# Performance work log

Measured on AMD Instinct MI355X. Metric: run time of the kernel, lower is better.

Reference implementation:

```python
import jax, jax.numpy as jnp
import numpy as np

N = 16384      # query points
XD = 3         # coord dims
CD = 2         # conditioning dims
E = 4          # experts
M = 2048       # memory entries per expert
D3 = 128       # feature_dim_3d (= key_dim)
D1 = 64        # feature_dim_1d
HE = 256       # encoder mlp hidden
HM = 256       # final mlp hidden
RES = 64       # line resolution (cond_hidden_dims)
TOPK_MEM = 16  # top_K memory entries
NF = 10        # positional-encoding frequencies
OMEGA = 30.0   # siren frequency


def pos_enc(c):
    # NeRF PE, torch ordering: coords, then per-freq per-dim (sin, cos)
    outs = [c]
    for i in range(NF):
        for j in range(XD):
            a = (2.0 ** i) * np.pi * c[:, j]
            outs.append(jnp.sin(a)[:, None])
            outs.append(jnp.cos(a)[:, None])
    return jnp.concatenate(outs, axis=-1)  # [N, 63]


def layernorm(h, g, b, eps=1e-5):
    mu = jnp.mean(h, axis=-1, keepdims=True)
    var = jnp.var(h, axis=-1, keepdims=True)
    return (h - mu) * jax.lax.rsqrt(var + eps) * g + b


def setup_inputs() -> dict:
    key = jax.random.key(0)
    ks = jax.random.split(key, 32)
    nrm = lambda i, shape, s: jax.random.normal(ks[i], shape, dtype=jnp.float32) * s
    inp = {}
    inp['x'] = jax.random.uniform(ks[0], (N, XD + CD), dtype=jnp.float32)
    # lines: U(0.01**0.5, 0.02**0.5) per torch init (len(line_dimid)=2)
    inp['lines'] = jax.random.uniform(ks[1], (CD, D1, RES), minval=0.1, maxval=0.1414, dtype=jnp.float32)
    # manager net
    inp['Wm1'] = nrm(2, (XD, 64), 0.5)
    inp['bm1'] = jnp.zeros((64,), jnp.float32)
    inp['Wm2'] = nrm(3, (64, E), 0.5)
    inp['bm2'] = jnp.zeros((E,), jnp.float32)
    # per-expert siren encoder (xavier-ish)
    inp['We1'] = nrm(4, (E, 63, HE), (2.0 / (63 + HE)) ** 0.5)
    inp['be1'] = jnp.zeros((E, HE), jnp.float32)
    inp['We2'] = nrm(5, (E, HE, HE), (1.0 / HE) ** 0.5)
    inp['be2'] = jnp.zeros((E, HE), jnp.float32)
    inp['We3'] = nrm(6, (E, HE, D3), (2.0 / (HE + D3)) ** 0.5)
    inp['be3'] = jnp.zeros((E, D3), jnp.float32)
    # shared layernorm on query features
    inp['ln_g'] = jnp.ones((D3,), jnp.float32)
    inp['ln_b'] = jnp.zeros((D3,), jnp.float32)
    # per-expert cross attention
    s = D3 ** -0.5
    inp['Wq'] = nrm(7, (E, D3, D3), s)
    inp['Wk'] = nrm(8, (E, D3, D3), s)
    inp['Wv'] = nrm(9, (E, D3, D3), s)
    inp['A1'] = nrm(10, (E, D3 + D1, 64), (2.0 / (D3 + D1 + 64)) ** 0.5)
    inp['a1'] = nrm(11, (E, 64), 0.001)
    inp['A2'] = nrm(12, (E, 64, D3), (2.0 / (64 + D3)) ** 0.5)
    inp['a2'] = nrm(13, (E, D3), 0.001)
    inp['aln_g'] = jnp.ones((E, D3), jnp.float32)
    inp['aln_b'] = jnp.zeros((E, D3), jnp.float32)
    # memory banks: keys kaiming-ish, values U(-1e-3, 1e-3)
    inp['mem_k'] = nrm(14, (E, M, D3), (2.0 / D3) ** 0.5)
    inp['mem_v'] = jax.random.uniform(ks[15], (E, M, D3), minval=-0.001, maxval=0.001, dtype=jnp.float32)
    # final mlp
    inp['M1'] = nrm(16, (D3, HM), (2.0 / (D3 + HM)) ** 0.5)
    inp['c1'] = nrm(17, (HM,), 0.001)
    inp['M2'] = nrm(18, (HM, HM), (2.0 / (HM + HM)) ** 0.5)
    inp['c2'] = nrm(19, (HM,), 0.001)
    inp['M3'] = nrm(20, (HM, HM), (2.0 / (HM + HM)) ** 0.5)
    inp['c3'] = nrm(21, (HM,), 0.001)
    inp['M4'] = nrm(22, (HM, 1), (2.0 / (HM + 1)) ** 0.5)
    inp['c4'] = nrm(23, (1,), 0.001)
    inp['top_k'] = 2
    return inp


def reference(x, lines, Wm1, bm1, Wm2, bm2, We1, be1, We2, be2, We3, be3,
              ln_g, ln_b, Wq, Wk, Wv, A1, a1, A2, a2, aln_g, aln_b,
              mem_k, mem_v, M1, c1, M2, c2, M3, c3, M4, c4, top_k):
    coords = x[:, :XD]
    # --- 1D line feature product (param_feats) ---
    pf = jnp.ones((D1, x.shape[0]), x.dtype)
    for i in range(CD):
        p = x[:, XD + i] * (RES - 1)
        f = jnp.floor(p)
        w = p - f
        i0 = f.astype(jnp.int32)
        i1 = jnp.clip(f + 1.0, 0.0, RES - 1).astype(jnp.int32)
        a = lines[i][:, i0]          # [D1, N]
        b = lines[i][:, i1]
        pf = pf * (a + w * (b - a))  # torch.lerp
    param_feats = pf.T               # [N, D1]
    # --- manager gating ---
    logits = jax.nn.relu(coords @ Wm1 + bm1) @ Wm2 + bm2
    probs = jax.nn.softmax(logits, axis=-1)
    gvals, gidx = jax.lax.top_k(probs, top_k)
    gvals = gvals / jnp.sum(gvals, axis=-1, keepdims=True)
    pe = pos_enc(coords)             # [N, 63]
    scale = D3 ** 0.5
    spatial = jnp.zeros((x.shape[0], D3), x.dtype)
    for e in range(E):
        # siren encoder
        h = jnp.sin(OMEGA * (pe @ We1[e] + be1[e]))
        h = jnp.sin(OMEGA * (h @ We2[e] + be2[e]))
        feats = h @ We3[e] + be3[e]                      # [N, D3]
        q = layernorm(feats, ln_g, ln_b)
        Q = q @ Wq[e]                                    # [N, D3]
        K = mem_k[e] @ Wk[e]                             # [M, D3]
        V = mem_v[e] @ Wv[e]
        # chunked topk over unscaled scores == global topk (chunk_size >= top_K)
        scores = Q @ K.T                                 # [N, M]
        _, ti = jax.lax.top_k(scores, TOPK_MEM)          # [N, k]
        Kt = K[ti]                                       # [N, k, D3]
        Vt = V[ti]
        pf_b = jnp.broadcast_to(param_feats[:, None, :], (Vt.shape[0], TOPK_MEM, D1))
        ain = jnp.concatenate([Vt, pf_b], axis=-1)       # [N, k, D3+D1]
        ad = jax.nn.relu(ain @ A1[e] + a1[e]) @ A2[e] + a2[e]
        Va = Vt + layernorm(ad, aln_g[e], aln_b[e])
        attn = jax.nn.softmax(jnp.einsum('nd,nkd->nk', Q, Kt) / scale, axis=-1)
        out_e = jnp.einsum('nk,nkd->nd', attn, Va) + feats
        w_e = jnp.sum(jnp.where(gidx == e, gvals, 0.0), axis=-1)  # routing weight
        spatial = spatial + w_e[:, None] * out_e
    h = jax.nn.relu(spatial @ M1 + c1)
    h = jax.nn.relu(h @ M2 + c2)
    h = jax.nn.relu(h @ M3 + c3)
    return jax.nn.sigmoid(h @ M4 + c4)
```

## Files before the change

### kernel.cpp

```cpp
#include <hip/hip_runtime.h>
#include <hip/hip_bf16.h>
#include <math.h>

#define NPTS 16384
#define NE 4
#define NM 2048
#define DD 128
#define DP 64
#define NHE 256
#define NHM 256
#define NRES 64
#define NTK 16
#define NEG_INF -3.402823466e38f

typedef unsigned short u16;
typedef __attribute__((ext_vector_type(8))) short short8;
typedef __attribute__((ext_vector_type(4))) float f32x4;

__device__ __forceinline__ u16 f2bf(float x) {
  union { float f; unsigned u; } v; v.f = x;
  unsigned r = v.u + 0x7fffu + ((v.u >> 16) & 1u);
  return (u16)(r >> 16);
}
__device__ __forceinline__ float bf2f(u16 b) {
  union { float f; unsigned u; } v; v.u = ((unsigned)b) << 16;
  return v.f;
}
__device__ __forceinline__ u16 bf2mono(u16 b) {
  return (u16)(b ^ ((b & 0x8000u) ? 0xFFFFu : 0x8000u));
}
__device__ __forceinline__ u16 mono2bf(u16 m) {
  return (u16)((m & 0x8000u) ? (m ^ 0x8000u) : (m ^ 0xFFFFu));
}

__global__ __launch_bounds__(256) void k_preproc(
    const float* __restrict__ x, const float* __restrict__ lines,
    const float* __restrict__ Wm1, const float* __restrict__ bm1,
    const float* __restrict__ Wm2, const float* __restrict__ bm2,
    float* __restrict__ pf, float* __restrict__ pe,
    float* __restrict__ slotW, int* __restrict__ plist,
    int* __restrict__ pairE, int* __restrict__ pairS, int* __restrict__ cnt)
{
  int n = blockIdx.x * 256 + threadIdx.x;
  int lane = threadIdx.x & 63;
  float c0 = x[n*5+0], c1 = x[n*5+1], c2 = x[n*5+2];

  float l0 = bm2[0], l1 = bm2[1], l2 = bm2[2], l3 = bm2[3];
#pragma unroll 4
  for (int j = 0; j < 64; ++j) {
    float h = fmaf(c0, Wm1[j], fmaf(c1, Wm1[64+j], fmaf(c2, Wm1[128+j], bm1[j])));
    h = fmaxf(h, 0.f);
    l0 = fmaf(h, Wm2[j*4+0], l0);
    l1 = fmaf(h, Wm2[j*4+1], l1);
    l2 = fmaf(h, Wm2[j*4+2], l2);
    l3 = fmaf(h, Wm2[j*4+3], l3);
  }
  float lg[4] = {l0, l1, l2, l3};
  float mx = fmaxf(fmaxf(l0, l1), fmaxf(l2, l3));
  float pr[4]; float ssum = 0.f;
#pragma unroll
  for (int k = 0; k < 4; ++k) { pr[k] = expf(lg[k] - mx); ssum += pr[k]; }
#pragma unroll
  for (int k = 0; k < 4; ++k) pr[k] /= ssum;
  int i0 = 0;
#pragma unroll
  for (int k = 1; k < 4; ++k) if (pr[k] > pr[i0]) i0 = k;
  int i1 = (i0 == 0) ? 1 : 0;
#pragma unroll
  for (int k = 0; k < 4; ++k) if (k != i0 && pr[k] > pr[i1]) i1 = k;
  float g0 = pr[i0], g1 = pr[i1], gs = g0 + g1;
  g0 /= gs; g1 /= gs;

  int s0 = 0, s1 = 0;
  unsigned long long below = (1ull << lane) - 1ull;
#pragma unroll
  for (int ee = 0; ee < 4; ++ee) {
    unsigned long long m0 = __ballot(i0 == ee);
    unsigned long long m1 = __ballot(i1 == ee);
    int tot = __popcll(m0) + __popcll(m1);
    int base = 0;
    if (lane == 0 && tot > 0) base = atomicAdd(&cnt[ee], tot);
    base = __shfl(base, 0);
    if (i0 == ee) s0 = base + __popcll(m0 & below);
    if (i1 == ee) s1 = base + __popcll(m0) + __popcll(m1 & below);
  }
  plist[i0*NPTS + s0] = n; slotW[i0*NPTS + s0] = g0;
  plist[i1*NPTS + s1] = n; slotW[i1*NPTS + s1] = g1;
  pairE[n*2+0] = i0; pairE[n*2+1] = i1;
  pairS[n*2+0] = s0; pairS[n*2+1] = s1;

  pe[(size_t)n*64 + 0] = c0;
  pe[(size_t)n*64 + 1] = c1;
  pe[(size_t)n*64 + 2] = c2;
  float cc[3] = {c0, c1, c2};
#pragma unroll
  for (int i = 0; i < 10; ++i) {
    float sc = 3.14159274101257324f * (float)(1 << i);
#pragma unroll
    for (int j = 0; j < 3; ++j) {
      float a = sc * cc[j];
      pe[(size_t)n*64 + 3 + (i*3+j)*2 + 0] = sinf(a);
      pe[(size_t)n*64 + 3 + (i*3+j)*2 + 1] = cosf(a);
    }
  }
  pe[(size_t)n*64 + 63] = 0.f;

  float pfv[64];
#pragma unroll
  for (int d = 0; d < 64; ++d) pfv[d] = 1.f;
  for (int i = 0; i < 2; ++i) {
    float p = x[n*5 + 3 + i] * 63.0f;
    float f = floorf(p);
    float wfr = p - f;
    int j0 = (int)f;
    int j1 = (int)fminf(f + 1.0f, 63.0f);
    const float* L = lines + (size_t)i * 64 * 64;
#pragma unroll
    for (int d = 0; d < 64; ++d) {
      float a = L[d*64 + j0];
      float b = L[d*64 + j1];
      pfv[d] *= a + wfr * (b - a);
    }
  }
#pragma unroll
  for (int d = 0; d < 64; ++d) pf[(size_t)n*64 + d] = pfv[d];
}

__global__ __launch_bounds__(256) void k_kv(
    const float* __restrict__ mem_k, const float* __restrict__ mem_v,
    const float* __restrict__ Wk, const float* __restrict__ Wv,
    u16* __restrict__ Khf, float* __restrict__ Vhat)
{
  int e = blockIdx.y;
  int which = blockIdx.z;
  const float* src = which ? mem_v : mem_k;
  const float* W   = which ? Wv : Wk;
  int r0 = blockIdx.x * 32;
  __shared__ float sm[32][130];
  int tid = threadIdx.x;
  for (int idx = tid; idx < 32*32; idx += 256) {
    int r = idx >> 5, c4 = (idx & 31) * 4;
    float4 v = *(const float4*)(src + ((size_t)e*NM + r0 + r)*DD + c4);
    sm[r][c4+0] = v.x; sm[r][c4+1] = v.y; sm[r][c4+2] = v.z; sm[r][c4+3] = v.w;
  }
  __syncthreads();
  int r = tid >> 3, cb = (tid & 7) * 16;
  float acc[16];
#pragma unroll
  for (int i = 0; i < 16; ++i) acc[i] = 0.f;
  const float* We = W + (size_t)e*DD*DD;
#pragma unroll 4
  for (int k = 0; k < 128; ++k) {
    float s = sm[r][k];
    const float4* w4 = (const float4*)(We + (size_t)k*DD + cb);
#pragma unroll
    for (int q = 0; q < 4; ++q) {
      float4 wv = w4[q];
      acc[q*4+0] = fmaf(s, wv.x, acc[q*4+0]);
      acc[q*4+1] = fmaf(s, wv.y, acc[q*4+1]);
      acc[q*4+2] = fmaf(s, wv.z, acc[q*4+2]);
      acc[q*4+3] = fmaf(s, wv.w, acc[q*4+3]);
    }
  }
  if (which) {
    float* drow = Vhat + ((size_t)e*NM + r0 + r)*DD + cb;
#pragma unroll
    for (int i = 0; i < 16; ++i) drow[i] = acc[i];
  } else {
    int key = r0 + r;
    int T = key >> 4;
    int kr = key & 15;
#pragma unroll
    for (int b = 0; b < 2; ++b) {
      int k_off = cb + b*8;
      int kt = k_off >> 5;
      int lhi = (k_off >> 3) & 3;
      int lane_ = lhi*16 + kr;
      size_t dst = (((size_t)e*128 + T)*4 + kt)*512 + (size_t)lane_*8;
      unsigned ph[4];
#pragma unroll
      for (int p = 0; p < 4; ++p) {
        u16 h0 = f2bf(acc[b*8 + p*2 + 0]);
        u16 h1 = f2bf(acc[b*8 + p*2 + 1]);
        ph[p] = (unsigned)h0 | ((unsigned)h1 << 16);
      }
      *(uint4*)(Khf + dst) = make_uint4(ph[0], ph[1], ph[2], ph[3]);
    }
  }
}

__global__ __launch_bounds__(64) void k_pack(
    const float* __restrict__ We1, const float* __restrict__ We2,
    const float* __restrict__ We3, const float* __restrict__ Wq,
    const float* __restrict__ A1, const float* __restrict__ A2,
    u16* __restrict__ We1h, u16* __restrict__ We1l,
    u16* __restrict__ We2h, u16* __restrict__ We2l,
    u16* __restrict__ We3h, u16* __restrict__ We3l,
    u16* __restrict__ Wqh,  u16* __restrict__ Wql,
    u16* __restrict__ A1h,  u16* __restrict__ A1l,
    u16* __restrict__ A2h,  u16* __restrict__ A2l)
{
  int e = blockIdx.y;
  int f = blockIdx.x;
  int lane = threadIdx.x;
  int col = lane & 15, khalf = lane >> 4;
  const float* src; u16 *dh, *dl;
  int Krows, N, ks, ct;
  if (f < 32) {
    int fl = f;        src = We1 + (size_t)e*63*256;  Krows = 63;  N = 256;
    ks = fl >> 4; ct = fl & 15;
    dh = We1h + ((size_t)e*32  + fl)*512; dl = We1l + ((size_t)e*32  + fl)*512;
  } else if (f < 160) {
    int fl = f - 32;   src = We2 + (size_t)e*256*256; Krows = 256; N = 256;
    ks = fl >> 4; ct = fl & 15;
    dh = We2h + ((size_t)e*128 + fl)*512; dl = We2l + ((size_t)e*128 + fl)*512;
  } else if (f < 224) {
    int fl = f - 160;  src = We3 + (size_t)e*256*128; Krows = 256; N = 128;
    ks = fl >> 3; ct = fl & 7;
    dh = We3h + ((size_t)e*64  + fl)*512; dl = We3l + ((size_t)e*64  + fl)*512;
  } else if (f < 256) {
    int fl = f - 224;  src = Wq  + (size_t)e*128*128; Krows = 128; N = 128;
    ks = fl >> 3; ct = fl & 7;
    dh = Wqh  + ((size_t)e*32  + fl)*512; dl = Wql  + ((size_t)e*32  + fl)*512;
  } else if (f < 280) {
    int fl = f - 256;  src = A1  + (size_t)e*192*64;  Krows = 192; N = 64;
    ks = fl >> 2; ct = fl & 3;
    dh = A1h  + ((size_t)e*24  + fl)*512; dl = A1l  + ((size_t)e*24  + fl)*512;
  } else {
    int fl = f - 280;  src = A2  + (size_t)e*64*128;  Krows = 64;  N = 128;
    ks = fl >> 3; ct = fl & 7;
    dh = A2h  + ((size_t)e*16  + fl)*512; dl = A2l  + ((size_t)e*16  + fl)*512;
  }
  unsigned ph[4], pl[4];
#pragma unroll
  for (int p = 0; p < 4; ++p) {
    int k0 = ks*32 + khalf*8 + 2*p;
    float x0 = (k0   < Krows) ? src[(size_t)k0*N     + ct*16 + col] : 0.f;
    float x1 = (k0+1 < Krows) ? src[(size_t)(k0+1)*N + ct*16 + col] : 0.f;
    u16 h0 = f2bf(x0), h1 = f2bf(x1);
    u16 l0 = f2bf(x0 - bf2f(h0)), l1 = f2bf(x1 - bf2f(h1));
    ph[p] = (unsigned)h0 | ((unsigned)h1 << 16);
    pl[p] = (unsigned)l0 | ((unsigned)l1 << 16);
  }
  *(uint4*)(dh + lane*8) = make_uint4(ph[0], ph[1], ph[2], ph[3]);
  *(uint4*)(dl + lane*8) = make_uint4(pl[0], pl[1], pl[2], pl[3]);
}

__global__ __launch_bounds__(64) void k_packM(
    const float* __restrict__ M1, const float* __restrict__ M2,
    const float* __restrict__ M3,
    u16* __restrict__ M1h, u16* __restrict__ M1l,
    u16* __restrict__ M2h, u16* __restrict__ M2l,
    u16* __restrict__ M3h, u16* __restrict__ M3l)
{
  int f = blockIdx.x;
  int lane = threadIdx.x;
  int col = lane & 15, khalf = lane >> 4;
  const float* src; u16 *dh, *dl;
  int ks, ct;
  if (f < 64)       { int fl=f;     src=M1; ks=fl>>4; ct=fl&15; dh=M1h+(size_t)fl*512; dl=M1l+(size_t)fl*512; }
  else if (f < 192) { int fl=f-64;  src=M2; ks=fl>>4; ct=fl&15; dh=M2h+(size_t)fl*512; dl=M2l+(size_t)fl*512; }
  else              { int fl=f-192; src=M3; ks=fl>>4; ct=fl&15; dh=M3h+(size_t)fl*512; dl=M3l+(size_t)fl*512; }
  unsigned ph[4], pl[4];
#pragma unroll
  for (int p = 0; p < 4; ++p) {
    int k0 = ks*32 + khalf*8 + 2*p;
    float x0 = src[(size_t)k0*NHM     + ct*16 + col];
    float x1 = src[(size_t)(k0+1)*NHM + ct*16 + col];
    u16 h0 = f2bf(x0), h1 = f2bf(x1);
    u16 l0 = f2bf(x0 - bf2f(h0)), l1 = f2bf(x1 - bf2f(h1));
    ph[p] = (unsigned)h0 | ((unsigned)h1 << 16);
    pl[p] = (unsigned)l0 | ((unsigned)l1 << 16);
  }
  *(uint4*)(dh + lane*8) = make_uint4(ph[0], ph[1], ph[2], ph[3]);
  *(uint4*)(dl + lane*8) = make_uint4(pl[0], pl[1], pl[2], pl[3]);
}

#define CONV_FRAG(PTR, AH, AL) {                                        \
    const float* p_ = (PTR);                                            \
    float4 u0_ = *(const float4*)p_, u1_ = *(const float4*)(p_+4);      \
    float xv_[8] = {u0_.x,u0_.y,u0_.z,u0_.w,u1_.x,u1_.y,u1_.z,u1_.w};   \
    union { unsigned u[4]; short8 s; } H_, L_;                          \
    _Pragma("unroll")                                                   \
    for (int q_ = 0; q_ < 4; ++q_) {                                    \
      u16 h0_ = f2bf(xv_[2*q_]), h1_ = f2bf(xv_[2*q_+1]);               \
      u16 l0_ = f2bf(xv_[2*q_] - bf2f(h0_));                            \
      u16 l1_ = f2bf(xv_[2*q_+1] - bf2f(h1_));                          \
      H_.u[q_] = (unsigned)h0_ | ((unsigned)h1_ << 16);                 \
      L_.u[q_] = (unsigned)l0_ | ((unsigned)l1_ << 16);                 \
    }                                                                   \
    AH = H_.s; AL = L_.s; }

__global__ __launch_bounds__(256) void k_expert(
    const float* __restrict__ pe,
    const u16* __restrict__ We1h, const u16* __restrict__ We1l,
    const u16* __restrict__ We2h, const u16* __restrict__ We2l,
    const u16* __restrict__ We3h, const u16* __restrict__ We3l,
    const u16* __restrict__ Wqh,  const u16* __restrict__ Wql,
    const float* __restrict__ be1, const float* __restrict__ be2,
    const float* __restrict__ be3,
    const float* __restrict__ ln_g, const float* __restrict__ ln_b,
    const int* __restrict__ plist, const int* __restrict__ cnt,
    float* __restrict__ featsC, float* __restrict__ QC)
{
  int e = blockIdx.y;
  int count = cnt[e];
  int base = blockIdx.x * 32;
  if (base >= count) return;
  __shared__ float actA[16*512];
  __shared__ float lnS[256];
  __shared__ int pts[32];
  int tid = threadIdx.x;
  int w = tid >> 6, lane = tid & 63;
  int rloc = lane & 15, khalf = lane >> 4;

  if (tid < 32) {
    int slot = base + tid;
    pts[tid] = (slot < count) ? plist[e*NPTS + slot] : 0;
  } else if (tid >= 64 && tid < 192) {
    int i = tid - 64;
    lnS[i] = ln_g[i];
    lnS[128 + i] = ln_b[i];
  }
  __syncthreads();
  {
    int Mt = tid >> 7, ks = (tid >> 6) & 1;
    const float* src = pe + (size_t)pts[Mt*16 + rloc]*64 + ks*32 + khalf*8;
    float4 a = *(const float4*)src;
    float4 b = *(const float4*)(src + 4);
    float* d = &actA[(Mt*8 + ks)*512 + lane*8];
    *(float4*)d = a; *(float4*)(d + 4) = b;
  }
  __syncthreads();

  {
    f32x4 acc[2][4];
#pragma unroll
    for (int Mt = 0; Mt < 2; ++Mt)
#pragma unroll
      for (int c = 0; c < 4; ++c) acc[Mt][c] = (f32x4){0.f,0.f,0.f,0.f};
    for (int ks = 0; ks < 2; ++ks) {
      short8 ah[2], al[2];
#pragma unroll
      for (int Mt = 0; Mt < 2; ++Mt)
        CONV_FRAG(&actA[(Mt*8+ks)*512 + lane*8], ah[Mt], al[Mt]);
#pragma unroll
      for (int c = 0; c < 4; ++c) {
        size_t fo = ((size_t)e*32 + ks*16 + w*4 + c)*512 + (size_t)lane*8;
        short8 bh = *(const short8*)(We1h + fo);
        short8 bl = *(const short8*)(We1l + fo);
#pragma unroll
        for (int Mt = 0; Mt < 2; ++Mt) {
          acc[Mt][c] = __builtin_amdgcn_mfma_f32_16x16x32_bf16(ah[Mt], bh, acc[Mt][c], 0,0,0);
          acc[Mt][c] = __builtin_amdgcn_mfma_f32_16x16x32_bf16(ah[Mt], bl, acc[Mt][c], 0,0,0);
          acc[Mt][c] = __builtin_amdgcn_mfma_f32_16x16x32_bf16(al[Mt], bh, acc[Mt][c], 0,0,0);
        }
      }
    }
    __syncthreads();
#pragma unroll
    for (int Mt = 0; Mt < 2; ++Mt)
#pragma unroll
      for (int c = 0; c < 4; ++c) {
        int n = (w*4+c)*16 + rloc;
        float b = be1[e*NHE + n];
        int ksp = n >> 5, lp = ((n>>3)&3)*16, jp = n & 7;
#pragma unroll
        for (int i = 0; i < 4; ++i)
          actA[(Mt*8+ksp)*512 + (lp + khalf*4 + i)*8 + jp] = sinf(30.f*(acc[Mt][c][i] + b));
      }
    __syncthreads();
  }

  {
    f32x4 acc[2][4];
#pragma unroll
    for (int Mt = 0; Mt < 2; ++Mt)
#pragma unroll
      for (int c = 0; c < 4; ++c) acc[Mt][c] = (f32x4){0.f,0.f,0.f,0.f};
#pragma unroll 2
    for (int ks = 0; ks < 8; ++ks) {
      short8 ah[2], al[2];
#pragma unroll
      for (int Mt = 0; Mt < 2; ++Mt)
        CONV_FRAG(&actA[(Mt*8+ks)*512 + lane*8], ah[Mt], al[Mt]);
#pragma unroll
      for (int c = 0; c < 4; ++c) {
        size_t fo = ((size_t)e*128 + ks*16 + w*4 + c)*512 + (size_t)lane*8;
        short8 bh = *(const short8*)(We2h + fo);
        short8 bl = *(const short8*)(We2l + fo);
#pragma unroll
        for (int Mt = 0; Mt < 2; ++Mt) {
          acc[Mt][c] = __builtin_amdgcn_mfma_f32_16x16x32_bf16(ah[Mt], bh, acc[Mt][c], 0,0,0);
          acc[Mt][c] = __builtin_amdgcn_mfma_f32_16x16x32_bf16(ah[Mt], bl, acc[Mt][c], 0,0,0);
          acc[Mt][c] = __builtin_amdgcn_mfma_f32_16x16x32_bf16(al[Mt], bh, acc[Mt][c], 0,0,0);
        }
      }
    }
    __syncthreads();
#pragma unroll
    for (int Mt = 0; Mt < 2; ++Mt)
#pragma unroll
      for (int c = 0; c < 4; ++c) {
        int n = (w*4+c)*16 + rloc;
        float b = be2[e*NHE + n];
        int ksp = n >> 5, lp = ((n>>3)&3)*16, jp = n & 7;
#pragma unroll
        for (int i = 0; i < 4; ++i)
          actA[(Mt*8+ksp)*512 + (lp + khalf*4 + i)*8 + jp] = sinf(30.f*(acc[Mt][c][i] + b));
      }
    __syncthreads();
  }

  {
    f32x4 acc[2][2];
#pragma unroll
    for (int Mt = 0; Mt < 2; ++Mt)
#pragma unroll
      for (int c = 0; c < 2; ++c) acc[Mt][c] = (f32x4){0.f,0.f,0.f,0.f};
#pragma unroll 2
    for (int ks = 0; ks < 8; ++ks) {
      short8 ah[2], al[2];
#pragma unroll
      for (int Mt = 0; Mt < 2; ++Mt)
        CONV_FRAG(&actA[(Mt*8+ks)*512 + lane*8], ah[Mt], al[Mt]);
#pragma unroll
      for (int c = 0; c < 2; ++c) {
        size_t fo = ((size_t)e*64 + ks*8 + w*2 + c)*512 + (size_t)lane*8;
        short8 bh = *(const short8*)(We3h + fo);
        short8 bl = *(const short8*)(We3l + fo);
#pragma unroll
        for (int Mt = 0; Mt < 2; ++Mt) {
          acc[Mt][c] = __builtin_amdgcn_mfma_f32_16x16x32_bf16(ah[Mt], bh, acc[Mt][c], 0,0,0);
          acc[Mt][c] = __builtin_amdgcn_mfma_f32_16x16x32_bf16(ah[Mt], bl, acc[Mt][c], 0,0,0);
          acc[Mt][c] = __builtin_amdgcn_mfma_f32_16x16x32_bf16(al[Mt], bh, acc[Mt][c], 0,0,0);
        }
      }
    }
    __syncthreads();
#pragma unroll
    for (int Mt = 0; Mt < 2; ++Mt)
#pragma unroll
      for (int c = 0; c < 2; ++c) {
        int n = (w*2+c)*16 + rloc;
        float b = be3[e*DD + n];
        int ksp = n >> 5, lp = ((n>>3)&3)*16, jp = n & 7;
#pragma unroll
        for (int i = 0; i < 4; ++i) {
          float f = acc[Mt][c][i] + b;
          actA[(Mt*8+ksp)*512 + (lp + khalf*4 + i)*8 + jp] = f;
          int slot = base + Mt*16 + khalf*4 + i;
          if (slot < count)
            featsC[((size_t)e*NPTS + slot)*DD + n] = f;
        }
      }
    __syncthreads();
  }

  {
    float mu[2], rsv[2];
#pragma unroll
    for (int Mt = 0; Mt < 2; ++Mt) {
      float sm = 0.f, sq = 0.f;
#pragma unroll
      for (int ks = 0; ks < 4; ++ks) {
        const float* p = &actA[(Mt*8+ks)*512 + lane*8];
        float4 u0 = *(const float4*)p, u1 = *(const float4*)(p+4);
        sm += u0.x+u0.y+u0.z+u0.w + u1.x+u1.y+u1.z+u1.w;
        sq += u0.x*u0.x+u0.y*u0.y+u0.z*u0.z+u0.w*u0.w
            + u1.x*u1.x+u1.y*u1.y+u1.z*u1.z+u1.w*u1.w;
      }
      sm += __shfl_xor(sm, 16); sq += __shfl_xor(sq, 16);
      sm += __shfl_xor(sm, 32); sq += __shfl_xor(sq, 32);
      mu[Mt] = sm * (1.f/128.f);
      rsv[Mt] = rsqrtf(sq * (1.f/128.f) - mu[Mt]*mu[Mt] + 1e-5f);
    }
    f32x4 acc[2][2];
#pragma unroll
    for (int Mt = 0; Mt < 2; ++Mt)
#pragma unroll
      for (int c = 0; c < 2; ++c) acc[Mt][c] = (f32x4){0.f,0.f,0.f,0.f};
    for (int ks = 0; ks < 4; ++ks) {
      short8 ah[2], al[2];
#pragma unroll
      for (int Mt = 0; Mt < 2; ++Mt) {
        const float* p = &actA[(Mt*8+ks)*512 + lane*8];
        float4 u0 = *(const float4*)p, u1 = *(const float4*)(p+4);
        float xv[8] = {u0.x,u0.y,u0.z,u0.w,u1.x,u1.y,u1.z,u1.w};
        union { unsigned u[4]; short8 s; } H, L;
#pragma unroll
        for (int j = 0; j < 8; ++j) {
          int k = ks*32 + khalf*8 + j;
          xv[j] = (xv[j] - mu[Mt]) * rsv[Mt] * lnS[k] + lnS[128 + k];
        }
#pragma unroll
        for (int q = 0; q < 4; ++q) {
          u16 h0 = f2bf(xv[2*q]), h1 = f2bf(xv[2*q+1]);
          u16 l0 = f2bf(xv[2*q] - bf2f(h0)), l1 = f2bf(xv[2*q+1] - bf2f(h1));
          H.u[q] = (unsigned)h0 | ((unsigned)h1 << 16);
          L.u[q] = (unsigned)l0 | ((unsigned)l1 << 16);
        }
        ah[Mt] = H.s; al[Mt] = L.s;
      }
#pragma unroll
      for (int c = 0; c < 2; ++c) {
        size_t fo = ((size_t)e*32 + ks*8 + w*2 + c)*512 + (size_t)lane*8;
        short8 bh = *(const short8*)(Wqh + fo);
        short8 bl = *(const short8*)(Wql + fo);
#pragma unroll
        for (int Mt = 0; Mt < 2; ++Mt) {
          acc[Mt][c] = __builtin_amdgcn_mfma_f32_16x16x32_bf16(ah[Mt], bh, acc[Mt][c], 0,0,0);
          acc[Mt][c] = __builtin_amdgcn_mfma_f32_16x16x32_bf16(ah[Mt], bl, acc[Mt][c], 0,0,0);
          acc[Mt][c] = __builtin_amdgcn_mfma_f32_16x16x32_bf16(al[Mt], bh, acc[Mt][c], 0,0,0);
        }
      }
    }
#pragma unroll
    for (int Mt = 0; Mt < 2; ++Mt)
#pragma unroll
      for (int c = 0; c < 2; ++c) {
        int n = (w*2+c)*16 + rloc;
#pragma unroll
        for (int i = 0; i < 4; ++i) {
          int slot = base + Mt*16 + khalf*4 + i;
          if (slot < count)
            QC[((size_t)e*NPTS + slot)*DD + n] = acc[Mt][c][i];
        }
      }
  }
}

__global__ __launch_bounds__(512) void k_scores(
    const float* __restrict__ QC, const u16* __restrict__ Khf,
    const int* __restrict__ cnt,
    float* __restrict__ attnW, int* __restrict__ attnI)
{
  int e = blockIdx.y;
  int count = cnt[e];
  int sbase = blockIdx.x * 16;
  if (sbase >= count) return;
  __shared__ u16 Sall[16*2056];
  int tid = threadIdx.x;
  int w = tid >> 6, lane = tid & 63;
  int rloc = lane & 15, khalf = lane >> 4;

  short8 qf[4];
  {
    int slot = sbase + rloc;
    const float* Qr = QC + ((size_t)e*NPTS + slot)*DD + khalf*8;
#pragma unroll
    for (int kt = 0; kt < 4; ++kt) {
      float q[8];
      if (slot < count) {
#pragma unroll
        for (int i = 0; i < 8; ++i) q[i] = Qr[kt*32 + i];
      } else {
#pragma unroll
        for (int i = 0; i < 8; ++i) q[i] = 0.f;
      }
      union { u16 h[8]; short8 s; } U;
#pragma unroll
      for (int i = 0; i < 8; ++i) U.h[i] = f2bf(q[i]);
      qf[kt] = U.s;
    }
  }

  const u16* KhB = Khf + (size_t)e*128*4*512 + (size_t)lane*8;
  for (int it = 0; it < 16; ++it) {
    int T = it*8 + w;
    f32x4 acc = {0.f, 0.f, 0.f, 0.f};
#pragma unroll
    for (int kt = 0; kt < 4; ++kt) {
      short8 kf = *(const short8*)(KhB + ((size_t)T*4 + kt)*512);
      acc = __builtin_amdgcn_mfma_f32_16x16x32_bf16(kf, qf[kt], acc, 0, 0, 0);
    }
    union { u16 h[4]; ushort4 v; } P;
#pragma unroll
    for (int i = 0; i < 4; ++i) P.h[i] = bf2mono(f2bf(acc[i]));
    *(ushort4*)&Sall[(size_t)rloc*2056 + T*16 + khalf*4] = P.v;
  }
  __syncthreads();

  const float inv_scale = 0.08838834764831845f;
#define INS4S(SL, P) { unsigned P_ = (P); if (P_ > p3[SL]) { p3[SL] = P_;       \
      if (p3[SL] > p2[SL]) { unsigned t_=p2[SL]; p2[SL]=p3[SL]; p3[SL]=t_; }    \
      if (p2[SL] > p1[SL]) { unsigned t_=p1[SL]; p1[SL]=p2[SL]; p2[SL]=t_; }    \
      if (p1[SL] > p0[SL]) { unsigned t_=p0[SL]; p0[SL]=p1[SL]; p1[SL]=t_; } } }

  {
    const u16* Srow[2];
    unsigned p0[2], p1[2], p2[2], p3[2];
#pragma unroll
    for (int sl = 0; sl < 2; ++sl) {
      Srow[sl] = &Sall[(size_t)(w*2 + sl)*2056];
      p0[sl] = p1[sl] = p2[sl] = p3[sl] = 0;
    }
#pragma unroll
    for (int i = 0; i < 16; ++i) {
      int k0 = lane*2 + i*128;
      unsigned cw[2];
#pragma unroll
      for (int sl = 0; sl < 2; ++sl)
        cw[sl] = *(const unsigned*)(Srow[sl] + k0);
#pragma unroll
      for (int sl = 0; sl < 2; ++sl) {
        unsigned P0 = ((cw[sl] & 0xFFFFu) << 11) | (unsigned)(2047 - k0);
        unsigned P1 = ((cw[sl] >> 16) << 11)     | (unsigned)(2047 - (k0+1));
        INS4S(sl, P0);
        INS4S(sl, P1);
      }
    }
    unsigned keepP[2] = {0, 0};
    int popped[2] = {0, 0};
#pragma unroll 1
    for (int r = 0; r < 16; ++r) {
      unsigned m[2];
#pragma unroll
      for (int sl = 0; sl < 2; ++sl) m[sl] = p0[sl];
#pragma unroll
      for (int d = 1; d < 64; d <<= 1) {
#pragma unroll
        for (int sl = 0; sl < 2; ++sl) {
          unsigned o = __shfl_xor(m[sl], d);
          m[sl] = (o > m[sl]) ? o : m[sl];
        }
      }
#pragma unroll
      for (int sl = 0; sl < 2; ++sl) {
        if (lane == r) keepP[sl] = m[sl];
        if (p0[sl] == m[sl]) {
          p0[sl] = p1[sl]; p1[sl] = p2[sl]; p2[sl] = p3[sl]; p3[sl] = 0;
          if (++popped[sl] == 4) {
            p0[sl] = p1[sl] = p2[sl] = p3[sl] = 0;
            for (int i2 = 0; i2 < 16; ++i2) {
              int k0 = lane*2 + i2*128;
              unsigned cw = *(const unsigned*)(Srow[sl] + k0);
              unsigned P0 = ((cw & 0xFFFFu) << 11) | (unsigned)(2047 - k0);
              unsigned P1 = ((cw >> 16) << 11)     | (unsigned)(2047 - (k0+1));
              if (P0 < m[sl]) INS4S(sl, P0);
              if (P1 < m[sl]) INS4S(sl, P1);
            }
            popped[sl] = 0;
          }
        }
      }
    }
#pragma unroll
    for (int sl = 0; sl < 2; ++sl) {
      int slot = sbase + w*2 + sl;
      if (slot >= count) continue;
      int keyv = 2047 - (int)(keepP[sl] & 0x7FFu);
      float val = bf2f(mono2bf((u16)(keepP[sl] >> 11)));
      float m0 = __shfl(val, 0);
      float ev = expf((val - m0) * inv_scale);
      float sum = ev;
      sum += __shfl_xor(sum, 1); sum += __shfl_xor(sum, 2);
      sum += __shfl_xor(sum, 4); sum += __shfl_xor(sum, 8);
      if (lane < 16) {
        size_t off = ((size_t)e*NPTS + slot)*NTK + lane;
        attnW[off] = ev / sum;
        attnI[off] = keyv;
      }
    }
  }
#undef INS4S
}

__global__ __launch_bounds__(256) void k_adapter(
    const float* __restrict__ Vhat, const float* __restrict__ pf,
    const u16* __restrict__ A1h, const u16* __restrict__ A1l,
    const u16* __restrict__ A2h, const u16* __restrict__ A2l,
    const float* __restrict__ a1, const float* __restrict__ a2,
    const float* __restrict__ alng, const float* __restrict__ alnb,
    const float* __restrict__ attnW, const int* __restrict__ attnI,
    const float* __restrict__ featsC, const float* __restrict__ slotW,
    const int* __restrict__ plist, const int* __restrict__ cnt,
    float* __restrict__ outC)
{
  int e = blockIdx.y;
  int count = cnt[e];
  int s0 = blockIdx.x * 4;
  if (s0 >= count) return;
  __shared__ float ainV[64][132];
  __shared__ float hid[64][68];
  __shared__ float pfS[4][68];
  __shared__ float attwS[4][16];
  __shared__ float alnS[128], albS[128];
  __shared__ int   rtiS[64];
  __shared__ float wslS[4];
  __shared__ int   ptlS[4];
  int tid = threadIdx.x;
  if (tid < 64) {
    int sl = tid >> 4, key = tid & 15;
    int slot = s0 + sl;
    if (slot < count) {
      size_t o = ((size_t)e*NPTS + slot)*NTK + key;
      rtiS[tid] = attnI[o];
      attwS[sl][key] = attnW[o];
    } else { rtiS[tid] = 0; attwS[sl][key] = 0.f; }
  } else if (tid < 68) {
    int sl = tid - 64;
    int slot = s0 + sl;
    wslS[sl] = (slot < count) ? slotW[e*NPTS + slot] : 0.f;
    ptlS[sl] = (slot < count) ? plist[e*NPTS + slot] : 0;
  } else if (tid >= 128 && tid < 192) {
    int c2 = (tid - 128) * 2;
    alnS[c2]   = alng[e*DD + c2];
    alnS[c2+1] = alng[e*DD + c2+1];
    albS[c2]   = alnb[e*DD + c2];
    albS[c2+1] = alnb[e*DD + c2+1];
  }
  __syncthreads();
  for (int idx = tid; idx < 64*32; idx += 256) {
    int r = idx >> 5, c4 = (idx & 31) * 4;
    *(float4*)&ainV[r][c4] = *(const float4*)(Vhat + ((size_t)e*NM + rtiS[r])*DD + c4);
  }
  if (tid < 64) {
    int sl = tid >> 4, c4 = (tid & 15) * 4;
    *(float4*)&pfS[sl][c4] = *(const float4*)(pf + (size_t)ptlS[sl]*64 + c4);
  }
  __syncthreads();

  int w = tid >> 6, lane = tid & 63;
  int rloc = lane & 15;
  int khalf = lane >> 4;

  f32x4 acc1[4];
#pragma unroll
  for (int ct = 0; ct < 4; ++ct) acc1[ct] = (f32x4){0.f, 0.f, 0.f, 0.f};
  for (int ks = 0; ks < 6; ++ks) {
    short8 ah, al;
    {
      const float* src = (ks < 4) ? &ainV[w*16 + rloc][ks*32 + khalf*8]
                                  : &pfS[w][(ks-4)*32 + khalf*8];
      CONV_FRAG(src, ah, al);
    }
    const u16* bh0 = A1h + ((size_t)e*24 + ks*4)*512 + (size_t)lane*8;
    const u16* bl0 = A1l + ((size_t)e*24 + ks*4)*512 + (size_t)lane*8;
#pragma unroll
    for (int ct = 0; ct < 4; ++ct) {
      short8 bh = *(const short8*)(bh0 + ct*512);
      short8 bl = *(const short8*)(bl0 + ct*512);
      acc1[ct] = __builtin_amdgcn_mfma_f32_16x16x32_bf16(ah, bh, acc1[ct], 0, 0, 0);
      acc1[ct] = __builtin_amdgcn_mfma_f32_16x16x32_bf16(ah, bl, acc1[ct], 0, 0, 0);
      acc1[ct] = __builtin_amdgcn_mfma_f32_16x16x32_bf16(al, bh, acc1[ct], 0, 0, 0);
    }
  }
#pragma unroll
  for (int ct = 0; ct < 4; ++ct) {
    float b = a1[e*64 + ct*16 + rloc];
#pragma unroll
    for (int i = 0; i < 4; ++i)
      hid[w*16 + khalf*4 + i][ct*16 + rloc] = fmaxf(acc1[ct][i] + b, 0.f);
  }

  f32x4 acc2[8];
#pragma unroll
  for (int ct = 0; ct < 8; ++ct) acc2[ct] = (f32x4){0.f, 0.f, 0.f, 0.f};
  for (int ks = 0; ks < 2; ++ks) {
    short8 ah, al;
    CONV_FRAG(&hid[w*16 + rloc][ks*32 + khalf*8], ah, al);
    const u16* bh0 = A2h + ((size_t)e*16 + ks*8)*512 + (size_t)lane*8;
    const u16* bl0 = A2l + ((size_t)e*16 + ks*8)*512 + (size_t)lane*8;
#pragma unroll
    for (int ct = 0; ct < 8; ++ct) {
      short8 bh = *(const short8*)(bh0 + ct*512);
      short8 bl = *(const short8*)(bl0 + ct*512);
      acc2[ct] = __builtin_amdgcn_mfma_f32_16x16x32_bf16(ah, bh, acc2[ct], 0, 0, 0);
      acc2[ct] = __builtin_amdgcn_mfma_f32_16x16x32_bf16(ah, bl, acc2[ct], 0, 0, 0);
      acc2[ct] = __builtin_amdgcn_mfma_f32_16x16x32_bf16(al, bh, acc2[ct], 0, 0, 0);
    }
  }

  float ad[8][4];
#pragma unroll
  for (int ct = 0; ct < 8; ++ct) {
    float b = a2[e*DD + ct*16 + rloc];
#pragma unroll
    for (int i = 0; i < 4; ++i) ad[ct][i] = acc2[ct][i] + b;
  }
  float mu[4], rsv[4];
#pragma unroll
  for (int i = 0; i < 4; ++i) {
    float sm = 0.f, sq = 0.f;
#pragma unroll
    for (int ct = 0; ct < 8; ++ct) { sm += ad[ct][i]; sq += ad[ct][i]*ad[ct][i]; }
    sm += __shfl_xor(sm, 1); sq += __shfl_xor(sq, 1);
    sm += __shfl_xor(sm, 2); sq += __shfl_xor(sq, 2);
    sm += __shfl_xor(sm, 4); sq += __shfl_xor(sq, 4);
    sm += __shfl_xor(sm, 8); sq += __shfl_xor(sq, 8);
    mu[i] = sm * (1.f/128.f);
    float var = sq * (1.f/128.f) - mu[i]*mu[i];
    rsv[i] = rsqrtf(var + 1e-5f);
  }
  float aw[4];
#pragma unroll
  for (int i = 0; i < 4; ++i) aw[i] = attwS[w][khalf*4 + i];

  float outv[8];
#pragma unroll
  for (int ct = 0; ct < 8; ++ct) {
    int cg = ct*16 + rloc;
    float g = alnS[cg], bb = albS[cg];
    float s = 0.f;
#pragma unroll
    for (int i = 0; i < 4; ++i) {
      float vt = ainV[w*16 + khalf*4 + i][cg];
      s += aw[i] * (vt + (ad[ct][i] - mu[i]) * rsv[i] * g + bb);
    }
    outv[ct] = s;
  }
#pragma unroll
  for (int ct = 0; ct < 8; ++ct) {
    outv[ct] += __shfl_xor(outv[ct], 16);
    outv[ct] += __shfl_xor(outv[ct], 32);
  }
  int slot = s0 + w;
  if (khalf == 0 && slot < count) {
    size_t o = ((size_t)e*NPTS + slot)*DD;
    float wg = wslS[w];
#pragma unroll
    for (int ct = 0; ct < 8; ++ct) {
      int cg = ct*16 + rloc;
      outC[o + cg] = wg * (outv[ct] + featsC[o + cg]);
    }
  }
}

__global__ __launch_bounds__(256) void k_final(
    const float* __restrict__ outC, const int* __restrict__ pairE, const int* __restrict__ pairS,
    const u16* __restrict__ M1h, const u16* __restrict__ M1l,
    const u16* __restrict__ M2h, const u16* __restrict__ M2l,
    const u16* __restrict__ M3h, const u16* __restrict__ M3l,
    const float* __restrict__ c1, const float* __restrict__ c2,
    const float* __restrict__ c3,
    const float* __restrict__ M4, const float* __restrict__ c4,
    float* __restrict__ out)
{
  int base = blockIdx.x * 32;
  __shared__ float actA[16*512];
  __shared__ float M4S[256];
  __shared__ int prE[64], prS[64];
  int tid = threadIdx.x;
  int w = tid >> 6, lane = tid & 63;
  int rloc = lane & 15, khalf = lane >> 4;

  if (tid < 64) {
    prE[tid] = pairE[(size_t)base*2 + tid];
    prS[tid] = pairS[(size_t)base*2 + tid];
  } else if (tid >= 64 && tid < 128) {
    int i = (tid - 64) * 4;
    *(float4*)&M4S[i] = *(const float4*)(M4 + i);
  }
  __syncthreads();
#pragma unroll
  for (int it = 0; it < 2; ++it) {
    int combo = it*4 + w;
    int Mt = combo >> 2, ks = combo & 3;
    int row = Mt*16 + rloc;
    const float* sA = outC + ((size_t)prE[row*2+0]*NPTS + prS[row*2+0])*DD + ks*32 + khalf*8;
    const float* sB = outC + ((size_t)prE[row*2+1]*NPTS + prS[row*2+1])*DD + ks*32 + khalf*8;
    float4 a0 = *(const float4*)sA, a1 = *(const float4*)(sA+4);
    float4 b0 = *(const float4*)sB, b1 = *(const float4*)(sB+4);
    float* d = &actA[(Mt*8 + ks)*512 + lane*8];
    d[0]=a0.x+b0.x; d[1]=a0.y+b0.y; d[2]=a0.z+b0.z; d[3]=a0.w+b0.w;
    d[4]=a1.x+b1.x; d[5]=a1.y+b1.y; d[6]=a1.z+b1.z; d[7]=a1.w+b1.w;
  }
  __syncthreads();

  {
    f32x4 acc[2][4];
#pragma unroll
    for (int Mt = 0; Mt < 2; ++Mt)
#pragma unroll
      for (int c = 0; c < 4; ++c) acc[Mt][c] = (f32x4){0.f,0.f,0.f,0.f};
    for (int ks = 0; ks < 4; ++ks) {
      short8 ah[2], al[2];
#pragma unroll
      for (int Mt = 0; Mt < 2; ++Mt)
        CONV_FRAG(&actA[(Mt*8+ks)*512 + lane*8], ah[Mt], al[Mt]);
#pragma unroll
      for (int c = 0; c < 4; ++c) {
        size_t fo = ((size_t)(ks*16 + w*4 + c))*512 + (size_t)lane*8;
        short8 bh = *(const short8*)(M1h + fo);
        short8 bl = *(const short8*)(M1l + fo);
#pragma unroll
        for (int Mt = 0; Mt < 2; ++Mt) {
          acc[Mt][c] = __builtin_amdgcn_mfma_f32_16x16x32_bf16(ah[Mt], bh, acc[Mt][c], 0,0,0);
          acc[Mt][c] = __builtin_amdgcn_mfma_f32_16x16x32_bf16(ah[Mt], bl, acc[Mt][c], 0,0,0);
          acc[Mt][c] = __builtin_amdgcn_mfma_f32_16x16x32_bf16(al[Mt], bh, acc[Mt][c], 0,0,0);
        }
      }
    }
    __syncthreads();
#pragma unroll
    for (int Mt = 0; Mt < 2; ++Mt)
#pragma unroll
      for (int c = 0; c < 4; ++c) {
        int n = (w*4+c)*16 + rloc;
        float b = c1[n];
        int ksp = n >> 5, lp = ((n>>3)&3)*16, jp = n & 7;
#pragma unroll
        for (int i = 0; i < 4; ++i)
          actA[(Mt*8+ksp)*512 + (lp + khalf*4 + i)*8 + jp] = fmaxf(acc[Mt][c][i] + b, 0.f);
      }
    __syncthreads();
  }

#pragma unroll 1
  for (int layer = 0; layer < 2; ++layer) {
    const u16* Wh = layer ? M3h : M2h;
    const u16* Wl = layer ? M3l : M2l;
    const float* bias = layer ? c3 : c2;
    f32x4 acc[2][4];
#pragma unroll
    for (int Mt = 0; Mt < 2; ++Mt)
#pragma unroll
      for (int c = 0; c < 4; ++c) acc[Mt][c] = (f32x4){0.f,0.f,0.f,0.f};
#pragma unroll 2
    for (int ks = 0; ks < 8; ++ks) {
      short8 ah[2], al[2];
#pragma unroll
      for (int Mt = 0; Mt < 2; ++Mt)
        CONV_FRAG(&actA[(Mt*8+ks)*512 + lane*8], ah[Mt], al[Mt]);
#pragma unroll
      for (int c = 0; c < 4; ++c) {
        size_t fo = ((size_t)(ks*16 + w*4 + c))*512 + (size_t)lane*8;
        short8 bh = *(const short8*)(Wh + fo);
        short8 bl = *(const short8*)(Wl + fo);
#pragma unroll
        for (int Mt = 0; Mt < 2; ++Mt) {
          acc[Mt][c] = __builtin_amdgcn_mfma_f32_16x16x32_bf16(ah[Mt], bh, acc[Mt][c], 0,0,0);
          acc[Mt][c] = __builtin_amdgcn_mfma_f32_16x16x32_bf16(ah[Mt], bl, acc[Mt][c], 0,0,0);
          acc[Mt][c] = __builtin_amdgcn_mfma_f32_16x16x32_bf16(al[Mt], bh, acc[Mt][c], 0,0,0);
        }
      }
    }
    __syncthreads();
#pragma unroll
    for (int Mt = 0; Mt < 2; ++Mt)
#pragma unroll
      for (int c = 0; c < 4; ++c) {
        int n = (w*4+c)*16 + rloc;
        float b = bias[n];
        int ksp = n >> 5, lp = ((n>>3)&3)*16, jp = n & 7;
#pragma unroll
        for (int i = 0; i < 4; ++i)
          actA[(Mt*8+ksp)*512 + (lp + khalf*4 + i)*8 + jp] = fmaxf(acc[Mt][c][i] + b, 0.f);
      }
    __syncthreads();
  }

  if (w < 2) {
    int Mt = w;
    float p = 0.f;
#pragma unroll
    for (int ks = 0; ks < 8; ++ks) {
      const float* pp = &actA[(Mt*8+ks)*512 + lane*8];
      const float* mm = &M4S[ks*32 + khalf*8];
#pragma unroll
      for (int j = 0; j < 8; ++j) p = fmaf(pp[j], mm[j], p);
    }
    p += __shfl_xor(p, 16);
    p += __shfl_xor(p, 32);
    if (khalf == 0) {
      float z = p + c4[0];
      out[base + Mt*16 + rloc] = 1.f / (1.f + expf(-z));
    }
  }
}

extern "C" void kernel_launch(void* const* d_in, const int* in_sizes, int n_in,
                              void* d_out, int out_size, void* d_ws, size_t ws_size,
                              hipStream_t stream)
{
  const float* x    = (const float*)d_in[0];
  const float* lines= (const float*)d_in[1];
  const float* Wm1  = (const float*)d_in[2];
  const float* bm1  = (const float*)d_in[3];
  const float* Wm2  = (const float*)d_in[4];
  const float* bm2  = (const float*)d_in[5];
  const float* We1  = (const float*)d_in[6];
  const float* be1  = (const float*)d_in[7];
  const float* We2  = (const float*)d_in[8];
  const float* be2  = (const float*)d_in[9];
  const float* We3  = (const float*)d_in[10];
  const float* be3  = (const float*)d_in[11];
  const float* ln_g = (const float*)d_in[12];
  const float* ln_b = (const float*)d_in[13];
  const float* Wq   = (const float*)d_in[14];
  const float* Wk   = (const float*)d_in[15];
  const float* Wv   = (const float*)d_in[16];
  const float* A1   = (const float*)d_in[17];
  const float* a1   = (const float*)d_in[18];
  const float* A2   = (const float*)d_in[19];
  const float* a2   = (const float*)d_in[20];
  const float* alng = (const float*)d_in[21];
  const float* alnb = (const float*)d_in[22];
  const float* mem_k= (const float*)d_in[23];
  const float* mem_v= (const float*)d_in[24];
  const float* M1   = (const float*)d_in[25];
  const float* c1   = (const float*)d_in[26];
  const float* M2   = (const float*)d_in[27];
  const float* c2   = (const float*)d_in[28];
  const float* M3   = (const float*)d_in[29];
  const float* c3   = (const float*)d_in[30];
  const float* M4   = (const float*)d_in[31];
  const float* c4   = (const float*)d_in[32];
  float* out = (float*)d_out;

  char* wp = (char*)d_ws;
  auto alloc = [&](size_t bytes) -> void* {
    void* p = (void*)wp;
    wp += (bytes + 255) & ~(size_t)255;
    return p;
  };
  float* pf     = (float*)alloc((size_t)NPTS*64*4);
  float* pe     = (float*)alloc((size_t)NPTS*64*4);
  u16*   Khf    = (u16*)alloc((size_t)NE*128*4*512*2);
  u16*   We1h   = (u16*)alloc((size_t)NE*32*512*2);
  u16*   We1l   = (u16*)alloc((size_t)NE*32*512*2);
  u16*   We2h   = (u16*)alloc((size_t)NE*128*512*2);
  u16*   We2l   = (u16*)alloc((size_t)NE*128*512*2);
  u16*   We3h   = (u16*)alloc((size_t)NE*64*512*2);
  u16*   We3l   = (u16*)alloc((size_t)NE*64*512*2);
  u16*   Wqh    = (u16*)alloc((size_t)NE*32*512*2);
  u16*   Wql    = (u16*)alloc((size_t)NE*32*512*2);
  u16*   A1h    = (u16*)alloc((size_t)NE*24*512*2);
  u16*   A1l    = (u16*)alloc((size_t)NE*24*512*2);
  u16*   A2h    = (u16*)alloc((size_t)NE*16*512*2);
  u16*   A2l    = (u16*)alloc((size_t)NE*16*512*2);
  u16*   M1h    = (u16*)alloc((size_t)64*512*2);
  u16*   M1l    = (u16*)alloc((size_t)64*512*2);
  u16*   M2h    = (u16*)alloc((size_t)128*512*2);
  u16*   M2l    = (u16*)alloc((size_t)128*512*2);
  u16*   M3h    = (u16*)alloc((size_t)128*512*2);
  u16*   M3l    = (u16*)alloc((size_t)128*512*2);
  float* Vhat   = (float*)alloc((size_t)NE*NM*DD*4);
  float* featsC = (float*)alloc((size_t)NE*NPTS*DD*4);
  float* QoutC  = (float*)alloc((size_t)NE*NPTS*DD*4);
  float* attnWb = (float*)alloc((size_t)NE*NPTS*NTK*4);
  float* slotW  = (float*)alloc((size_t)NE*NPTS*4);
  int*   attnIb = (int*)alloc((size_t)NE*NPTS*NTK*4);
  int*   plist  = (int*)alloc((size_t)NE*NPTS*4);
  int*   pairE  = (int*)alloc((size_t)NPTS*2*4);
  int*   pairS  = (int*)alloc((size_t)NPTS*2*4);
  int*   cnt    = (int*)alloc(64);

  hipMemsetAsync(cnt, 0, 64, stream);
  k_preproc<<<NPTS/256, 256, 0, stream>>>(x, lines, Wm1, bm1, Wm2, bm2,
                                          pf, pe, slotW, plist, pairE, pairS, cnt);
  k_kv<<<dim3(NM/32, NE, 2), 256, 0, stream>>>(mem_k, mem_v, Wk, Wv, Khf, Vhat);
  k_pack<<<dim3(296, NE), 64, 0, stream>>>(We1, We2, We3, Wq, A1, A2,
                                           We1h, We1l, We2h, We2l,
                                           We3h, We3l, Wqh, Wql,
                                           A1h, A1l, A2h, A2l);
  k_packM<<<320, 64, 0, stream>>>(M1, M2, M3, M1h, M1l, M2h, M2l, M3h, M3l);
  k_expert<<<dim3(NPTS/32, NE), 256, 0, stream>>>(pe, We1h, We1l, We2h, We2l,
                                                  We3h, We3l, Wqh, Wql,
                                                  be1, be2, be3, ln_g, ln_b,
                                                  plist, cnt, featsC, QoutC);
  k_scores<<<dim3(NPTS/16, NE), 512, 0, stream>>>(QoutC, Khf, cnt, attnWb, attnIb);
  k_adapter<<<dim3(NPTS/4, NE), 256, 0, stream>>>(Vhat, pf, A1h, A1l, A2h, A2l,
                                                  a1, a2, alng, alnb,
                                                  attnWb, attnIb, featsC, slotW, plist, cnt,
                                                  QoutC);
  k_final<<<NPTS/32, 256, 0, stream>>>(QoutC, pairE, pairS,
                                       M1h, M1l, M2h, M2l, M3h, M3l,
                                       c1, c2, c3, M4, c4, out);
}
```

Measured before the change: 521.8 us.

## Precompute V·A1 per memory entry and gather it in adapter kernel

The adapter's first layer splits into a V-part and a param-feature part. The V-part (Vt @ A1[:128]) depends only on the memory entry, so it is now computed once per entry (2048×4) in a new fp32 kernel instead of once per gathered (point, key) pair. The adapter gathers 64-wide precomputed rows and runs only the pf portion through MFMA, which cuts four of the six k-steps. The Vt values for the residual are now read straight from global memory rather than from shared memory, and one extra small kernel launch is added.

```diff
diff --git a/kernel.cpp b/kernel.cpp
--- a/kernel.cpp
+++ b/kernel.cpp
@@ -187,6 +187,44 @@
       *(uint4*)(Khf + dst) = make_uint4(ph[0], ph[1], ph[2], ph[3]);
     }
   }
+}
+
+__global__ __launch_bounds__(256) void k_va1(
+    const float* __restrict__ Vhat, const float* __restrict__ A1,
+    float* __restrict__ VA1)
+{
+  int e = blockIdx.y;
+  int r0 = blockIdx.x * 32;
+  __shared__ float sm[32][130];
+  int tid = threadIdx.x;
+  for (int idx = tid; idx < 32*32; idx += 256) {
+    int r = idx >> 5, c4 = (idx & 31) * 4;
+    float4 v = *(const float4*)(Vhat + ((size_t)e*NM + r0 + r)*DD + c4);
+    sm[r][c4+0] = v.x; sm[r][c4+1] = v.y; sm[r][c4+2] = v.z; sm[r][c4+3] = v.w;
+  }
+  __syncthreads();
+  int r = tid >> 3, cb = (tid & 7) * 8;
+  float acc[8];
+#pragma unroll
+  for (int i = 0; i < 8; ++i) acc[i] = 0.f;
+  const float* Ae = A1 + (size_t)e*192*64;
+#pragma unroll 4
+  for (int k = 0; k < 128; ++k) {
+    float s = sm[r][k];
+    const float4* w4 = (const float4*)(Ae + (size_t)k*64 + cb);
+    float4 w0 = w4[0], w1 = w4[1];
+    acc[0] = fmaf(s, w0.x, acc[0]);
+    acc[1] = fmaf(s, w0.y, acc[1]);
+    acc[2] = fmaf(s, w0.z, acc[2]);
+    acc[3] = fmaf(s, w0.w, acc[3]);
+    acc[4] = fmaf(s, w1.x, acc[4]);
+    acc[5] = fmaf(s, w1.y, acc[5]);
+    acc[6] = fmaf(s, w1.z, acc[6]);
+    acc[7] = fmaf(s, w1.w, acc[7]);
+  }
+  float* dst = VA1 + ((size_t)e*NM + r0 + r)*64 + cb;
+  *(float4*)dst = make_float4(acc[0], acc[1], acc[2], acc[3]);
+  *(float4*)(dst+4) = make_float4(acc[4], acc[5], acc[6], acc[7]);
 }
 
 __global__ __launch_bounds__(64) void k_pack(
@@ -668,6 +706,7 @@
 
 __global__ __launch_bounds__(256) void k_adapter(
     const float* __restrict__ Vhat, const float* __restrict__ pf,
+    const float* __restrict__ VA1,
     const u16* __restrict__ A1h, const u16* __restrict__ A1l,
     const u16* __restrict__ A2h, const u16* __restrict__ A2l,
     const float* __restrict__ a1, const float* __restrict__ a2,
@@ -681,8 +720,8 @@
   int count = cnt[e];
   int s0 = blockIdx.x * 4;
   if (s0 >= count) return;
-  __shared__ float ainV[64][132];
   __shared__ float hid[64][68];
+  __shared__ float vaS[64][68];
   __shared__ float pfS[4][68];
   __shared__ float attwS[4][16];
   __shared__ float alnS[128], albS[128];
@@ -711,9 +750,9 @@
     albS[c2+1] = alnb[e*DD + c2+1];
   }
   __syncthreads();
-  for (int idx = tid; idx < 64*32; idx += 256) {
-    int r = idx >> 5, c4 = (idx & 31) * 4;
-    *(float4*)&ainV[r][c4] = *(const float4*)(Vhat + ((size_t)e*NM + rtiS[r])*DD + c4);
+  for (int idx = tid; idx < 64*16; idx += 256) {
+    int r = idx >> 4, c4 = (idx & 15) * 4;
+    *(float4*)&vaS[r][c4] = *(const float4*)(VA1 + ((size_t)e*NM + rtiS[r])*64 + c4);
   }
   if (tid < 64) {
     int sl = tid >> 4, c4 = (tid & 15) * 4;
@@ -728,13 +767,9 @@
   f32x4 acc1[4];
 #pragma unroll
   for (int ct = 0; ct < 4; ++ct) acc1[ct] = (f32x4){0.f, 0.f, 0.f, 0.f};
-  for (int ks = 0; ks < 6; ++ks) {
+  for (int ks = 4; ks < 6; ++ks) {
     short8 ah, al;
-    {
-      const float* src = (ks < 4) ? &ainV[w*16 + rloc][ks*32 + khalf*8]
-                                  : &pfS[w][(ks-4)*32 + khalf*8];
-      CONV_FRAG(src, ah, al);
-    }
+    CONV_FRAG(&pfS[w][(ks-4)*32 + khalf*8], ah, al);
     const u16* bh0 = A1h + ((size_t)e*24 + ks*4)*512 + (size_t)lane*8;
     const u16* bl0 = A1l + ((size_t)e*24 + ks*4)*512 + (size_t)lane*8;
 #pragma unroll
@@ -750,8 +785,10 @@
   for (int ct = 0; ct < 4; ++ct) {
     float b = a1[e*64 + ct*16 + rloc];
 #pragma unroll
-    for (int i = 0; i < 4; ++i)
-      hid[w*16 + khalf*4 + i][ct*16 + rloc] = fmaxf(acc1[ct][i] + b, 0.f);
+    for (int i = 0; i < 4; ++i) {
+      int row = w*16 + khalf*4 + i;
+      hid[row][ct*16 + rloc] = fmaxf(acc1[ct][i] + b + vaS[row][ct*16 + rloc], 0.f);
+    }
   }
 
   f32x4 acc2[8];
@@ -797,6 +834,11 @@
 #pragma unroll
   for (int i = 0; i < 4; ++i) aw[i] = attwS[w][khalf*4 + i];
 
+  const float* vrow[4];
+#pragma unroll
+  for (int i = 0; i < 4; ++i)
+    vrow[i] = Vhat + ((size_t)e*NM + rtiS[w*16 + khalf*4 + i])*DD;
+
   float outv[8];
 #pragma unroll
   for (int ct = 0; ct < 8; ++ct) {
@@ -805,7 +847,7 @@
     float s = 0.f;
 #pragma unroll
     for (int i = 0; i < 4; ++i) {
-      float vt = ainV[w*16 + khalf*4 + i][cg];
+      float vt = vrow[i][cg];
       s += aw[i] * (vt + (ad[ct][i] - mu[i]) * rsv[i] * g + bb);
     }
     outv[ct] = s;
@@ -1037,6 +1079,7 @@
   u16*   M3h    = (u16*)alloc((size_t)128*512*2);
   u16*   M3l    = (u16*)alloc((size_t)128*512*2);
   float* Vhat   = (float*)alloc((size_t)NE*NM*DD*4);
+  float* VA1    = (float*)alloc((size_t)NE*NM*64*4);
   float* featsC = (float*)alloc((size_t)NE*NPTS*DD*4);
   float* QoutC  = (float*)alloc((size_t)NE*NPTS*DD*4);
   float* attnWb = (float*)alloc((size_t)NE*NPTS*NTK*4);
@@ -1051,6 +1094,7 @@
   k_preproc<<<NPTS/256, 256, 0, stream>>>(x, lines, Wm1, bm1, Wm2, bm2,
                                           pf, pe, slotW, plist, pairE, pairS, cnt);
   k_kv<<<dim3(NM/32, NE, 2), 256, 0, stream>>>(mem_k, mem_v, Wk, Wv, Khf, Vhat);
+  k_va1<<<dim3(NM/32, NE), 256, 0, stream>>>(Vhat, A1, VA1);
   k_pack<<<dim3(296, NE), 64, 0, stream>>>(We1, We2, We3, Wq, A1, A2,
                                            We1h, We1l, We2h, We2l,
                                            We3h, We3l, Wqh, Wql,
@@ -1061,7 +1105,7 @@
                                                   be1, be2, be3, ln_g, ln_b,
                                                   plist, cnt, featsC, QoutC);
   k_scores<<<dim3(NPTS/16, NE), 512, 0, stream>>>(QoutC, Khf, cnt, attnWb, attnIb);
-  k_adapter<<<dim3(NPTS/4, NE), 256, 0, stream>>>(Vhat, pf, A1h, A1l, A2h, A2l,
+  k_adapter<<<dim3(NPTS/4, NE), 256, 0, stream>>>(Vhat, pf, VA1, A1h, A1l, A2h, A2l,
                                                   a1, a2, alng, alnb,
                                                   attnWb, attnIb, featsC, slotW, plist, cnt,
                                                   QoutC);
```

Result: faster. 468.0 us (-10.3%).
